# Optimization experiments

Hardware: AMD Instinct MI355X
Metric: run time of the kernel (lower is better)

Reference implementation:

```python
import jax, jax.numpy as jnp
import numpy as np

EPS = 1.0 / 137.0  # fine-structure-constant epsilon used throughout the Yat ops


def yat_dense(x, W, b, alpha):
    # x: [..., C], W: [C, F] -> [..., F]
    dot = jnp.einsum('btc,cf->btf', x, W)
    x_norm = jnp.sum(x * x, axis=-1, keepdims=True)        # [..., 1]
    w_norm = jnp.sum(W * W, axis=0)                         # [F]
    dist = x_norm + w_norm - 2.0 * dot
    y = dot * dot / (dist + EPS)
    y = y + b
    F = W.shape[1]
    scale = (np.sqrt(F) / np.log(1.0 + F)) ** 1.0           # base; alpha exponent applied below
    return y * ((np.float32(np.sqrt(F)) / np.float32(np.log1p(F))) ** alpha)


def setup_inputs() -> dict:
    key = jax.random.key(0)
    ks = jax.random.split(key, 8)
    B, T, C = 4, 1024, 768
    x = jax.random.normal(ks[0], (B, T, C), dtype=jnp.float32)
    mask = jnp.tril(jnp.ones((T, T), dtype=bool))[None, None, :, :]  # causal [1,1,T,T]
    sd = 1.0 / np.sqrt(C)
    W_attn = jax.random.normal(ks[1], (C, 3 * C), dtype=jnp.float32) * sd
    b_attn = jnp.zeros((3 * C,), dtype=jnp.float32)
    alpha_attn = jnp.ones((), dtype=jnp.float32)
    W_proj = jax.random.normal(ks[2], (C, C), dtype=jnp.float32) * sd
    b_proj = jnp.zeros((C,), dtype=jnp.float32)
    alpha_proj = jnp.ones((), dtype=jnp.float32)
    return {"x": x, "mask": mask, "W_attn": W_attn, "b_attn": b_attn,
            "alpha_attn": alpha_attn, "W_proj": W_proj, "b_proj": b_proj,
            "alpha_proj": alpha_proj}


def reference(x, mask, W_attn, b_attn, alpha_attn, W_proj, b_proj, alpha_proj):
    B, T, C = x.shape
    H = 12
    D = C // H  # head_dim
    qkv = yat_dense(x, W_attn, b_attn, alpha_attn)          # [B,T,3C]
    qkv = qkv.reshape(B, T, 3 * H, D)
    q, k, v = jnp.array_split(qkv, 3, axis=2)
    q = jnp.transpose(q, (0, 2, 1, 3))                       # [B,H,T,D]
    k = jnp.transpose(k, (0, 2, 1, 3))
    v = jnp.transpose(v, (0, 2, 1, 3))
    scale = 1.0 / np.float32(np.sqrt(D))
    dot = jnp.einsum('bhid,bhjd->bhij', q, k)                # [B,H,T,T]
    sq_dot = jnp.square(dot * scale)
    q_norm = jnp.sum(jnp.square(q), axis=-1)[..., None]      # [B,H,T,1]
    k_norm = jnp.sum(jnp.square(k), axis=-1)[..., None, :]   # [B,H,1,T]
    sq_dist = q_norm + k_norm - 2.0 * dot * scale
    attn = sq_dot / (sq_dist + EPS)
    attn = jnp.where(mask, attn, jnp.finfo(jnp.float32).min)
    attn = jax.nn.softmax(attn, axis=-1)
    out = jnp.einsum('bhij,bhjd->bhid', attn, v)             # [B,H,T,D]
    out = jnp.transpose(out, (0, 2, 1, 3)).reshape(B, T, C)
    out = yat_dense(out, W_proj, b_proj, alpha_proj)         # [B,T,C]
    return out
```

## Files before the change

### kernel.cpp

```cpp
#include <hip/hip_runtime.h>
#include <math.h>

#define EPS_YAT (1.0f/137.0f)

typedef unsigned short u16;
typedef unsigned int u32;
typedef __attribute__((ext_vector_type(8))) __bf16 bf16x8;
typedef __attribute__((ext_vector_type(4))) float f32x4;

__device__ __forceinline__ float4 ld4(const float* p) { return *(const float4*)p; }

__device__ __forceinline__ u16 bf16_rne(float f) {
    u32 u = __float_as_uint(f);
    u32 r = (u + 0x7fffu + ((u >> 16) & 1u)) >> 16;
    return (u16)r;
}
__device__ __forceinline__ float bf16_f(u16 h) {
    return __uint_as_float(((u32)h) << 16);
}

__device__ __forceinline__ void glds16(const u16* g, u16* s) {
    __builtin_amdgcn_global_load_lds(
        (const __attribute__((address_space(1))) void*)g,
        (__attribute__((address_space(3))) void*)s,
        16, 0, 0);
}

__global__ void colnorm_part2(const float* __restrict__ Wa, const float* __restrict__ Wp,
                              float* __restrict__ pa, float* __restrict__ pp) {
    __shared__ float sm[256];
    const float* W; float* part; int N, colbase;
    if (blockIdx.x < 36) { W = Wa; part = pa; N = 2304; colbase = blockIdx.x * 64; }
    else                 { W = Wp; part = pp; N = 768;  colbase = (blockIdx.x - 36) * 64; }
    const int col = colbase + (threadIdx.x & 63);
    const int q = threadIdx.x >> 6;
    const int k0 = blockIdx.y * 48 + q * 12;
    float s = 0.f;
    for (int k = k0; k < k0 + 12; ++k) {
        float w = W[(size_t)k * N + col];
        s += w * w;
    }
    sm[threadIdx.x] = s;
    __syncthreads();
    if (threadIdx.x < 64)
        part[(size_t)blockIdx.y * N + col] =
            sm[threadIdx.x] + sm[threadIdx.x + 64] + sm[threadIdx.x + 128] + sm[threadIdx.x + 192];
}

__global__ void colnorm_reduce2(const float* __restrict__ pa, const float* __restrict__ pp,
                                float* __restrict__ wa, float* __restrict__ wp,
                                float* __restrict__ an_zero) {
    int gid = blockIdx.x * 256 + threadIdx.x;
    if (gid < 2304) {
        float s = 0.f;
        #pragma unroll
        for (int i = 0; i < 16; ++i) s += pa[(size_t)i * 2304 + gid];
        wa[gid] = s;
    } else if (gid < 3072) {
        int g = gid - 2304;
        float s = 0.f;
        #pragma unroll
        for (int i = 0; i < 16; ++i) s += pp[(size_t)i * 768 + g];
        wp[g] = s;
    }
    int z = gid - 3072;
    if (z >= 0 && z < 4096) an_zero[z] = 0.f;
}

__global__ void split_rownorm(const float* __restrict__ X, u16* __restrict__ Xh,
                              u16* __restrict__ Xl, float* __restrict__ rn) {
    int wave = threadIdx.x >> 6;
    int lane = threadIdx.x & 63;
    int row = blockIdx.x * 4 + wave;
    const float* xr = X + (size_t)row * 768;
    u16* xh = Xh + (size_t)row * 768;
    u16* xl = Xl + (size_t)row * 768;
    float s = 0.f;
    #pragma unroll
    for (int k = lane * 4; k < 768; k += 256) {
        float4 v = ld4(xr + k);
        s += v.x * v.x + v.y * v.y + v.z * v.z + v.w * v.w;
        u16 h0 = bf16_rne(v.x), h1 = bf16_rne(v.y), h2 = bf16_rne(v.z), h3 = bf16_rne(v.w);
        u16 l0 = bf16_rne(v.x - bf16_f(h0));
        u16 l1 = bf16_rne(v.y - bf16_f(h1));
        u16 l2 = bf16_rne(v.z - bf16_f(h2));
        u16 l3 = bf16_rne(v.w - bf16_f(h3));
        uint2 hp, lp;
        hp.x = (u32)h0 | ((u32)h1 << 16); hp.y = (u32)h2 | ((u32)h3 << 16);
        lp.x = (u32)l0 | ((u32)l1 << 16); lp.y = (u32)l2 | ((u32)l3 << 16);
        *(uint2*)(xh + k) = hp;
        *(uint2*)(xl + k) = lp;
    }
    for (int off = 32; off; off >>= 1) s += __shfl_down(s, off);
    if (lane == 0) rn[row] = s;
}

__global__ void split_wt_kernel(const float* __restrict__ W, u16* __restrict__ Th,
                                u16* __restrict__ Tl, int K, int N) {
    __shared__ float tile[64 * 68];
    const int tid = threadIdx.x;
    const int n0 = blockIdx.x << 6;
    const int k0 = blockIdx.y << 6;
    const int rr = tid >> 4;
    const int cc = (tid & 15) << 2;
    #pragma unroll
    for (int s = 0; s < 4; ++s) {
        int k_l = rr + s * 16;
        *(float4*)&tile[k_l * 68 + cc] = ld4(W + (size_t)(k0 + k_l) * N + n0 + cc);
    }
    __syncthreads();
    #pragma unroll
    for (int s = 0; s < 4; ++s) {
        int n_l = rr + s * 16;
        float a0 = tile[(cc + 0) * 68 + n_l];
        float a1 = tile[(cc + 1) * 68 + n_l];
        float a2 = tile[(cc + 2) * 68 + n_l];
        float a3 = tile[(cc + 3) * 68 + n_l];
        u16 h0 = bf16_rne(a0), h1 = bf16_rne(a1), h2 = bf16_rne(a2), h3 = bf16_rne(a3);
        u16 l0 = bf16_rne(a0 - bf16_f(h0));
        u16 l1 = bf16_rne(a1 - bf16_f(h1));
        u16 l2 = bf16_rne(a2 - bf16_f(h2));
        u16 l3 = bf16_rne(a3 - bf16_f(h3));
        uint2 hp, lp;
        hp.x = (u32)h0 | ((u32)h1 << 16); hp.y = (u32)h2 | ((u32)h3 << 16);
        lp.x = (u32)l0 | ((u32)l1 << 16); lp.y = (u32)l2 | ((u32)l3 << 16);
        size_t o = (size_t)(n0 + n_l) * K + k0 + cc;
        *(uint2*)(Th + o) = hp;
        *(uint2*)(Tl + o) = lp;
    }
}

template<int SPLIT, int NB>
__global__ __launch_bounds__(256, 4)
void yat_gemm_mfma(const u16* __restrict__ Ah, const u16* __restrict__ Al,
                   const u16* __restrict__ Bh, const u16* __restrict__ Bl,
                   const float* __restrict__ bias, const float* __restrict__ xn,
                   const float* __restrict__ wnc, const float* __restrict__ alphap,
                   const float Fdim, float* __restrict__ out,
                   u16* __restrict__ outh, u16* __restrict__ outl,
                   float* __restrict__ qn, float* __restrict__ kn,
                   const int N, const int K) {
    __shared__ __align__(16) u16 lds[4096 + NB * 4096];
    const int tid = threadIdx.x;
    const int nwg = gridDim.x * gridDim.y;
    const int orig = blockIdx.y * gridDim.x + blockIdx.x;
    const int swz = (orig & 7) * (nwg >> 3) + (orig >> 3);
    const int m0 = (swz / gridDim.x) << 6;
    const int n0 = (swz % gridDim.x) * (64 * NB);
    const int w = tid >> 6;
    const int l = tid & 63;
    const int lm = l & 15;
    const int kq = l >> 4;
    const int kq4 = kq << 2;
    const int wn = w * 16 * NB;

    const int srow = (w << 4) + (l >> 2);
    const int scol = (l & 3) << 3;
    const u16* gA  = Ah + (size_t)(m0 + srow) * K + scol;
    const u16* gC  = Al + (size_t)(m0 + srow) * K + scol;
    const u16* gB  = Bh + (size_t)(n0 + srow) * K + scol;
    const u16* gD  = Bl + (size_t)(n0 + srow) * K + scol;
    const u16* gB2 = Bh + (size_t)(n0 + 64 + srow) * K + scol;
    const u16* gD2 = Bl + (size_t)(n0 + 64 + srow) * K + scol;
    const int wb = w << 9;

    u16* sAh = lds;
    u16* sAl = lds + 2048;
    u16* sBh = lds + 4096;
    u16* sBl = lds + 4096 + 2048 * NB;

    f32x4 acc[4][NB] = {};

    for (int k0 = 0; k0 < K; k0 += 32) {
        __syncthreads();
        glds16(gA + k0, sAh + wb);
        glds16(gC + k0, sAl + wb);
        glds16(gB + k0, sBh + wb);
        glds16(gD + k0, sBl + wb);
        if constexpr (NB == 2) {
            glds16(gB2 + k0, sBh + 2048 + wb);
            glds16(gD2 + k0, sBl + 2048 + wb);
        }
        __syncthreads();

        bf16x8 fah[4], fal[4], fbh[NB], fbl[NB];
        #pragma unroll
        for (int i = 0; i < 4; ++i) {
            const int ra = (i * 16 + lm) * 32 + (kq << 3);
            fah[i] = *(const bf16x8*)&sAh[ra];
            fal[i] = *(const bf16x8*)&sAl[ra];
        }
        #pragma unroll
        for (int j = 0; j < NB; ++j) {
            const int rb = (wn + j * 16 + lm) * 32 + (kq << 3);
            fbh[j] = *(const bf16x8*)&sBh[rb];
            fbl[j] = *(const bf16x8*)&sBl[rb];
        }
        #pragma unroll
        for (int i = 0; i < 4; ++i)
            #pragma unroll
            for (int j = 0; j < NB; ++j) {
                f32x4 c = acc[i][j];
                c = __builtin_amdgcn_mfma_f32_16x16x32_bf16(fah[i], fbh[j], c, 0, 0, 0);
                c = __builtin_amdgcn_mfma_f32_16x16x32_bf16(fah[i], fbl[j], c, 0, 0, 0);
                c = __builtin_amdgcn_mfma_f32_16x16x32_bf16(fal[i], fbh[j], c, 0, 0, 0);
                acc[i][j] = c;
            }
    }

    const float scale = powf(sqrtf(Fdim) / log1pf(Fdim), *alphap);
    float pp[4][4];
    #pragma unroll
    for (int i = 0; i < 4; ++i) {
        const int mbase = m0 + i * 16 + kq4;
        #pragma unroll
        for (int r = 0; r < 4; ++r) pp[i][r] = 0.f;
        #pragma unroll
        for (int j = 0; j < NB; ++j) {
            const int n = n0 + wn + j * 16 + lm;
            const float w2 = wnc[n];
            const float bv = bias[n];
            #pragma unroll
            for (int r = 0; r < 4; ++r) {
                const int m = mbase + r;
                float d = acc[i][j][r];
                float den = xn[m] + w2 - 2.f * d + EPS_YAT;
                float v = (d * d / den + bv) * scale;
                if constexpr (SPLIT) {
                    u16 hh = bf16_rne(v);
                    outh[(size_t)m * N + n] = hh;
                    outl[(size_t)m * N + n] = bf16_rne(v - bf16_f(hh));
                    pp[i][r] += v * v;
                } else {
                    out[(size_t)m * N + n] = v;
                }
            }
        }
    }

    if constexpr (SPLIT) {
        if (n0 < 1536) {
            __syncthreads();
            float* red = (float*)lds;
            #pragma unroll
            for (int i = 0; i < 4; ++i)
                #pragma unroll
                for (int r = 0; r < 4; ++r) {
                    float s = pp[i][r];
                    s += __shfl_xor(s, 1, 16);
                    s += __shfl_xor(s, 2, 16);
                    s += __shfl_xor(s, 4, 16);
                    s += __shfl_xor(s, 8, 16);
                    if (lm == 0) red[w * 64 + i * 16 + kq4 + r] = s;
                }
            __syncthreads();
            if (tid < 128) {
                const int hh = tid >> 6;
                const int ml = tid & 63;
                const float s = red[(2 * hh) * 64 + ml] + red[(2 * hh + 1) * 64 + ml];
                const int m = m0 + ml;
                const int b = m >> 10, t = m & 1023;
                const int hcol = n0 + hh * 64;
                if (hcol < 768)
                    qn[(b * 12 + (hcol >> 6)) * 1024 + t] = s;
                else
                    kn[(b * 12 + ((hcol - 768) >> 6)) * 1024 + t] = s;
            }
        }
    }
}

#define MFMA_B16(a, b, c) __builtin_amdgcn_mfma_f32_16x16x32_bf16(a, b, c, 0, 0, 0)

#define ST_TILE(j) { \
    const int kro = ((j)*16 + lm) * 72 + (kq << 3); \
    bf16x8 kh = *(const bf16x8*)&KPh[kro]; \
    bf16x8 kl = *(const bf16x8*)&KPl[kro]; \
    st##j = MFMA_B16(kh, qh0, st##j); \
    st##j = MFMA_B16(kl, qh0, st##j); \
    st##j = MFMA_B16(kh, ql0, st##j); \
    kh = *(const bf16x8*)&KPh[kro + 32]; \
    kl = *(const bf16x8*)&KPl[kro + 32]; \
    st##j = MFMA_B16(kh, qh1, st##j); \
    st##j = MFMA_B16(kl, qh1, st##j); \
    st##j = MFMA_B16(kh, ql1, st##j); \
}

#define YAT_EL(j, r) { \
    float sv = st##j[r] * 0.125f; \
    float den = qnm + kns[(j)*16 + kq4 + (r)] - 2.f * sv + EPS_YAT; \
    float v = sv * sv / den; \
    if (diag && ((j)*16 + kq4 + (r) > wband + lm)) v = -3e38f; \
    st##j[r] = v; mm = fmaxf(mm, v); }
#define YAT_TILE(j) YAT_EL(j,0) YAT_EL(j,1) YAT_EL(j,2) YAT_EL(j,3)

#define PEXP_TILE(j) { \
    float p0 = __expf(st##j[0] - mnew), p1 = __expf(st##j[1] - mnew); \
    float p2 = __expf(st##j[2] - mnew), p3 = __expf(st##j[3] - mnew); \
    rs += p0 + p1 + p2 + p3; \
    u16 h0 = bf16_rne(p0), h1 = bf16_rne(p1), h2 = bf16_rne(p2), h3 = bf16_rne(p3); \
    uint2 hp; hp.x = (u32)h0 | ((u32)h1 << 16); hp.y = (u32)h2 | ((u32)h3 << 16); \
    *(uint2*)&KPh[pmrow + (j)*16 + kq4] = hp; \
    u16 e0 = bf16_rne(p0 - bf16_f(h0)), e1 = bf16_rne(p1 - bf16_f(h1)); \
    u16 e2 = bf16_rne(p2 - bf16_f(h2)), e3 = bf16_rne(p3 - bf16_f(h3)); \
    uint2 lp; lp.x = (u32)e0 | ((u32)e1 << 16); lp.y = (u32)e2 | ((u32)e3 << 16); \
    *(uint2*)&KPl[pmrow + (j)*16 + kq4] = lp; }

#define PV_TILE(j) { \
    const int vro = ((j)*16 + lm) * 72 + vkq8; \
    bf16x8 vh = *(const bf16x8*)&Vth[vro]; \
    bf16x8 vl = *(const bf16x8*)&Vtl[vro]; \
    ac##j = MFMA_B16(ph0, vh, ac##j); \
    ac##j = MFMA_B16(pl0, vh, ac##j); \
    ac##j = MFMA_B16(ph0, vl, ac##j); \
    vh = *(const bf16x8*)&Vth[vro + 32]; \
    vl = *(const bf16x8*)&Vtl[vro + 32]; \
    ac##j = MFMA_B16(ph1, vh, ac##j); \
    ac##j = MFMA_B16(pl1, vh, ac##j); \
    ac##j = MFMA_B16(ph1, vl, ac##j); \
}

#define WRVT(dst, v2, m) { \
    dst[(sj * 4 + 16 * (m) + 0) * 72 + toks] = (u16)((v2).x); \
    dst[(sj * 4 + 16 * (m) + 1) * 72 + toks] = (u16)((v2).x >> 16); \
    dst[(sj * 4 + 16 * (m) + 2) * 72 + toks] = (u16)((v2).y); \
    dst[(sj * 4 + 16 * (m) + 3) * 72 + toks] = (u16)((v2).y >> 16); }

__global__ __launch_bounds__(256, 2)
void yat_flash_mfma(const u16* __restrict__ qh_g, const u16* __restrict__ ql_g,
                    const float* __restrict__ qn, const float* __restrict__ kn,
                    u16* __restrict__ outh, u16* __restrict__ outl,
                    float* __restrict__ an_g) {
    __shared__ __align__(16) u16 KPh[64 * 72], KPl[64 * 72];
    __shared__ __align__(16) u16 Vth[64 * 72], Vtl[64 * 72];
    __shared__ float kns[64];

    const int tid = threadIdx.x;
    const int L = blockIdx.x;
    const int u = L / 48;
    const int qt = (u & 1) ? (u >> 1) : (15 - (u >> 1));
    const int bh = L % 48;
    const int h = bh % 12, b = bh / 12;
    const int wave = tid >> 6;
    const int lane = tid & 63;
    const int lm = lane & 15;
    const int kq = lane >> 4;
    const int kq4 = kq << 2;
    const int wband = wave << 4;
    const int sr = tid >> 2;
    const int sj = tid & 3;
    const int toks = sr ^ (sj << 3);
    const int vkq8 = (kq ^ (lm >> 2)) << 3;
    const size_t base = (size_t)(b * 1024) * 2304 + h * 64;

    {
        const size_t qoff = base + (size_t)((qt << 6) + sr) * 2304 + sj * 16;
        *(uint4*)&KPh[sr * 72 + sj * 16]     = *(const uint4*)(qh_g + qoff);
        *(uint4*)&KPh[sr * 72 + sj * 16 + 8] = *(const uint4*)(qh_g + qoff + 8);
        *(uint4*)&KPl[sr * 72 + sj * 16]     = *(const uint4*)(ql_g + qoff);
        *(uint4*)&KPl[sr * 72 + sj * 16 + 8] = *(const uint4*)(ql_g + qoff + 8);
    }
    const float qnm = qn[bh * 1024 + (qt << 6) + wband + lm];

    const size_t r0 = base + (size_t)sr * 2304;
    uint4 kh0 = *(const uint4*)(qh_g + r0 + 768 + sj * 16);
    uint4 kh1 = *(const uint4*)(qh_g + r0 + 768 + sj * 16 + 8);
    uint4 kl0 = *(const uint4*)(ql_g + r0 + 768 + sj * 16);
    uint4 kl1 = *(const uint4*)(ql_g + r0 + 768 + sj * 16 + 8);
    uint2 vh0 = *(const uint2*)(qh_g + r0 + 1536 + sj * 4);
    uint2 vh1 = *(const uint2*)(qh_g + r0 + 1536 + sj * 4 + 16);
    uint2 vh2 = *(const uint2*)(qh_g + r0 + 1536 + sj * 4 + 32);
    uint2 vh3 = *(const uint2*)(qh_g + r0 + 1536 + sj * 4 + 48);
    uint2 vl0 = *(const uint2*)(ql_g + r0 + 1536 + sj * 4);
    uint2 vl1 = *(const uint2*)(ql_g + r0 + 1536 + sj * 4 + 16);
    uint2 vl2 = *(const uint2*)(ql_g + r0 + 1536 + sj * 4 + 32);
    uint2 vl3 = *(const uint2*)(ql_g + r0 + 1536 + sj * 4 + 48);
    float knS = (tid < 64) ? kn[bh * 1024 + tid] : 0.f;

    __syncthreads();

    const int qrow = (wband + lm) * 72;
    const bf16x8 qh0 = *(const bf16x8*)&KPh[qrow + (kq << 3)];
    const bf16x8 qh1 = *(const bf16x8*)&KPh[qrow + 32 + (kq << 3)];
    const bf16x8 ql0 = *(const bf16x8*)&KPl[qrow + (kq << 3)];
    const bf16x8 ql1 = *(const bf16x8*)&KPl[qrow + 32 + (kq << 3)];

    f32x4 ac0 = {}, ac1 = {}, ac2 = {}, ac3 = {};
    float mrun = -3e38f, lrun = 0.f;
    const int pmrow = (wband + lm) * 72;

    for (int kt = 0; kt <= qt; ++kt) {
        __syncthreads();
        *(uint4*)&KPh[sr * 72 + sj * 16]     = kh0;
        *(uint4*)&KPh[sr * 72 + sj * 16 + 8] = kh1;
        *(uint4*)&KPl[sr * 72 + sj * 16]     = kl0;
        *(uint4*)&KPl[sr * 72 + sj * 16 + 8] = kl1;
        WRVT(Vth, vh0, 0) WRVT(Vth, vh1, 1) WRVT(Vth, vh2, 2) WRVT(Vth, vh3, 3)
        WRVT(Vtl, vl0, 0) WRVT(Vtl, vl1, 1) WRVT(Vtl, vl2, 2) WRVT(Vtl, vl3, 3)
        if (tid < 64) kns[tid] = knS;
        __syncthreads();

        if (kt < qt) {
            const size_t r = base + (size_t)(((kt + 1) << 6) + sr) * 2304;
            kh0 = *(const uint4*)(qh_g + r + 768 + sj * 16);
            kh1 = *(const uint4*)(qh_g + r + 768 + sj * 16 + 8);
            kl0 = *(const uint4*)(ql_g + r + 768 + sj * 16);
            kl1 = *(const uint4*)(ql_g + r + 768 + sj * 16 + 8);
            vh0 = *(const uint2*)(qh_g + r + 1536 + sj * 4);
            vh1 = *(const uint2*)(qh_g + r + 1536 + sj * 4 + 16);
            vh2 = *(const uint2*)(qh_g + r + 1536 + sj * 4 + 32);
            vh3 = *(const uint2*)(qh_g + r + 1536 + sj * 4 + 48);
            vl0 = *(const uint2*)(ql_g + r + 1536 + sj * 4);
            vl1 = *(const uint2*)(ql_g + r + 1536 + sj * 4 + 16);
            vl2 = *(const uint2*)(ql_g + r + 1536 + sj * 4 + 32);
            vl3 = *(const uint2*)(ql_g + r + 1536 + sj * 4 + 48);
            if (tid < 64) knS = kn[bh * 1024 + ((kt + 1) << 6) + tid];
        }

        f32x4 st0 = {}, st1 = {}, st2 = {}, st3 = {};
        __builtin_amdgcn_s_setprio(1);
        ST_TILE(0) ST_TILE(1) ST_TILE(2) ST_TILE(3)
        __builtin_amdgcn_s_setprio(0);
        __syncthreads();

        const bool diag = (kt == qt);
        float mm = -3e38f;
        YAT_TILE(0) YAT_TILE(1) YAT_TILE(2) YAT_TILE(3)
        mm = fmaxf(mm, __shfl_xor(mm, 16));
        mm = fmaxf(mm, __shfl_xor(mm, 32));
        const float mnew = fmaxf(mrun, mm);
        if (!__all(mm <= mrun)) {
            const float al = __expf(mrun - mnew);
            const float a0 = __shfl(al, kq4 + 0, 16);
            const float a1 = __shfl(al, kq4 + 1, 16);
            const float a2 = __shfl(al, kq4 + 2, 16);
            const float a3 = __shfl(al, kq4 + 3, 16);
            ac0[0] *= a0; ac0[1] *= a1; ac0[2] *= a2; ac0[3] *= a3;
            ac1[0] *= a0; ac1[1] *= a1; ac1[2] *= a2; ac1[3] *= a3;
            ac2[0] *= a0; ac2[1] *= a1; ac2[2] *= a2; ac2[3] *= a3;
            ac3[0] *= a0; ac3[1] *= a1; ac3[2] *= a2; ac3[3] *= a3;
            lrun *= al;
        }
        mrun = mnew;
        float rs = 0.f;
        PEXP_TILE(0) PEXP_TILE(1) PEXP_TILE(2) PEXP_TILE(3)
        rs += __shfl_xor(rs, 16);
        rs += __shfl_xor(rs, 32);
        lrun += rs;
        __syncthreads();

        const bf16x8 ph0 = *(const bf16x8*)&KPh[pmrow + (kq << 3)];
        const bf16x8 ph1 = *(const bf16x8*)&KPh[pmrow + 32 + (kq << 3)];
        const bf16x8 pl0 = *(const bf16x8*)&KPl[pmrow + (kq << 3)];
        const bf16x8 pl1 = *(const bf16x8*)&KPl[pmrow + 32 + (kq << 3)];
        __builtin_amdgcn_s_setprio(1);
        PV_TILE(0) PV_TILE(1) PV_TILE(2) PV_TILE(3)
        __builtin_amdgcn_s_setprio(0);
    }

    const float i0 = 1.f / __shfl(lrun, kq4 + 0, 16);
    const float i1 = 1.f / __shfl(lrun, kq4 + 1, 16);
    const float i2 = 1.f / __shfl(lrun, kq4 + 2, 16);
    const float i3 = 1.f / __shfl(lrun, kq4 + 3, 16);
    const size_t obase = (size_t)(b * 1024 + (qt << 6) + wband + kq4) * 768 + h * 64 + lm;
    u16* oph = outh + obase;
    u16* opl = outl + obase;
    float rsum0 = 0.f, rsum1 = 0.f, rsum2 = 0.f, rsum3 = 0.f;
    #define STORE_E(j, r, iv) { \
        float ov = ac##j[r] * iv; \
        rsum##r += ov * ov; \
        u16 hh = bf16_rne(ov); \
        oph[(size_t)(r) * 768 + (j)*16] = hh; \
        opl[(size_t)(r) * 768 + (j)*16] = bf16_rne(ov - bf16_f(hh)); }
    #define STORE_T(j) { STORE_E(j,0,i0) STORE_E(j,1,i1) STORE_E(j,2,i2) STORE_E(j,3,i3) }
    STORE_T(0) STORE_T(1) STORE_T(2) STORE_T(3)
    #undef STORE_T
    #undef STORE_E
    const int arow = b * 1024 + (qt << 6) + wband + kq4;
    #define REDROW(r) { \
        float s = rsum##r; \
        s += __shfl_xor(s, 1, 16); \
        s += __shfl_xor(s, 2, 16); \
        s += __shfl_xor(s, 4, 16); \
        s += __shfl_xor(s, 8, 16); \
        if (lm == 0) atomicAdd(&an_g[arow + (r)], s); }
    REDROW(0) REDROW(1) REDROW(2) REDROW(3)
    #undef REDROW
}

extern "C" void kernel_launch(void* const* d_in, const int* in_sizes, int n_in,
                              void* d_out, int out_size, void* d_ws, size_t ws_size,
                              hipStream_t stream) {
    const float* x          = (const float*)d_in[0];
    const float* W_attn     = (const float*)d_in[2];
    const float* b_attn     = (const float*)d_in[3];
    const float* alpha_attn = (const float*)d_in[4];
    const float* W_proj     = (const float*)d_in[5];
    const float* b_proj     = (const float*)d_in[6];
    const float* alpha_proj = (const float*)d_in[7];

    float* ws       = (float*)d_ws;
    u16*   qkvh     = (u16*)ws;
    u16*   qkvl     = (u16*)(ws + 4718592);
    float* xn       = ws + 12582912;
    float* an       = ws + 12587008;
    float* wn_attn  = ws + 12591104;
    float* wn_proj  = ws + 12593408;
    float* qn       = ws + 12594176;
    float* kn       = ws + 12643328;

    float* cn_part_a = ws + 9437184;
    float* cn_part_p = ws + 9437184 + 36864;
    u16* xh  = (u16*)(ws + 9437184);
    u16* xl  = (u16*)(ws + 11010048);
    u16* aoh = (u16*)(ws + 9437184);
    u16* aol = (u16*)(ws + 11010048);
    u16* wth = (u16*)d_out;
    u16* wtl = (u16*)d_out + 1769472;
    u16* wph = (u16*)(ws + 3145728);
    u16* wpl = (u16*)(ws + 3440640);

    colnorm_part2<<<dim3(48, 16), 256, 0, stream>>>(W_attn, W_proj, cn_part_a, cn_part_p);
    colnorm_reduce2<<<28, 256, 0, stream>>>(cn_part_a, cn_part_p, wn_attn, wn_proj, an);
    split_rownorm<<<1024, 256, 0, stream>>>(x, xh, xl, xn);
    split_wt_kernel<<<dim3(36, 12), 256, 0, stream>>>(W_attn, wth, wtl, 768, 2304);
    yat_gemm_mfma<1, 2><<<dim3(18, 64), 256, 0, stream>>>(
        xh, xl, wth, wtl, b_attn, xn, wn_attn, alpha_attn, 2304.f,
        nullptr, qkvh, qkvl, qn, kn, 2304, 768);
    yat_flash_mfma<<<768, 256, 0, stream>>>(qkvh, qkvl, qn, kn, aoh, aol, an);
    split_wt_kernel<<<dim3(12, 12), 256, 0, stream>>>(W_proj, wph, wpl, 768, 768);
    yat_gemm_mfma<0, 1><<<dim3(12, 64), 256, 0, stream>>>(
        aoh, aol, wph, wpl, b_proj, an, wn_proj, alpha_proj, 768.f,
        (float*)d_out, nullptr, nullptr, nullptr, nullptr, 768, 768);
}
```

Measured before the change: 248.0 us.

## Use 128x128 tiles with K=64 steps in QKV split-bf16 GEMM

The QKV GEMM moves from 64x128 tiles to 128x128 tiles, with each wave owning a 64x64 sub-tile. The K step grows from 32 to 64, which halves the number of barrier pairs and raises reuse of each loaded fragment. The q/k norm reduction now writes directly from each wave instead of going through shared memory, because each wave covers a full 64-column head. The trade-off is higher register pressure (launch bounds drop to 2 blocks per SM), fewer blocks in flight, and possible LDS bank conflicts with the 64-wide row stride.

```diff
diff --git a/kernel.cpp b/kernel.cpp
--- a/kernel.cpp
+++ b/kernel.cpp
@@ -130,8 +130,8 @@
     }
 }
 
-template<int SPLIT, int NB>
-__global__ __launch_bounds__(256, 4)
+template<int SPLIT, int BIG>
+__global__ __launch_bounds__(256, BIG ? 2 : 4)
 void yat_gemm_mfma(const u16* __restrict__ Ah, const u16* __restrict__ Al,
                    const u16* __restrict__ Bh, const u16* __restrict__ Bl,
                    const float* __restrict__ bias, const float* __restrict__ xn,
@@ -140,84 +140,90 @@
                    u16* __restrict__ outh, u16* __restrict__ outl,
                    float* __restrict__ qn, float* __restrict__ kn,
                    const int N, const int K) {
-    __shared__ __align__(16) u16 lds[4096 + NB * 4096];
+    constexpr int TM = BIG ? 128 : 64;
+    constexpr int TN = BIG ? 128 : 64;
+    constexpr int JN = BIG ? 4 : 1;
+    __shared__ __align__(16) u16 lds[(TM + TN) * 64 * 2];
     const int tid = threadIdx.x;
     const int nwg = gridDim.x * gridDim.y;
     const int orig = blockIdx.y * gridDim.x + blockIdx.x;
     const int swz = (orig & 7) * (nwg >> 3) + (orig >> 3);
-    const int m0 = (swz / gridDim.x) << 6;
-    const int n0 = (swz % gridDim.x) * (64 * NB);
+    const int m0 = (swz / gridDim.x) * TM;
+    const int n0 = (swz % gridDim.x) * TN;
     const int w = tid >> 6;
     const int l = tid & 63;
     const int lm = l & 15;
     const int kq = l >> 4;
     const int kq4 = kq << 2;
-    const int wn = w * 16 * NB;
-
-    const int srow = (w << 4) + (l >> 2);
-    const int scol = (l & 3) << 3;
-    const u16* gA  = Ah + (size_t)(m0 + srow) * K + scol;
-    const u16* gC  = Al + (size_t)(m0 + srow) * K + scol;
-    const u16* gB  = Bh + (size_t)(n0 + srow) * K + scol;
-    const u16* gD  = Bl + (size_t)(n0 + srow) * K + scol;
-    const u16* gB2 = Bh + (size_t)(n0 + 64 + srow) * K + scol;
-    const u16* gD2 = Bl + (size_t)(n0 + 64 + srow) * K + scol;
-    const int wb = w << 9;
+    const int WM = BIG ? ((w >> 1) << 6) : 0;
+    const int WN = BIG ? ((w & 1) << 6) : (w << 4);
+
+    const int lrow = l >> 3;
+    const int lchunk = (l & 7) << 3;
 
     u16* sAh = lds;
-    u16* sAl = lds + 2048;
-    u16* sBh = lds + 4096;
-    u16* sBl = lds + 4096 + 2048 * NB;
-
-    f32x4 acc[4][NB] = {};
-
-    for (int k0 = 0; k0 < K; k0 += 32) {
+    u16* sAl = lds + TM * 64;
+    u16* sBh = lds + 2 * TM * 64;
+    u16* sBl = lds + 2 * TM * 64 + TN * 64;
+
+    f32x4 acc[4][JN] = {};
+
+    for (int k0 = 0; k0 < K; k0 += 64) {
         __syncthreads();
-        glds16(gA + k0, sAh + wb);
-        glds16(gC + k0, sAl + wb);
-        glds16(gB + k0, sBh + wb);
-        glds16(gD + k0, sBl + wb);
-        if constexpr (NB == 2) {
-            glds16(gB2 + k0, sBh + 2048 + wb);
-            glds16(gD2 + k0, sBl + 2048 + wb);
+        #pragma unroll
+        for (int c = 0; c < TM / 32; ++c) {
+            const int r0w = (TM / 4) * w + 8 * c;
+            const size_t go = (size_t)(m0 + r0w + lrow) * K + k0 + lchunk;
+            glds16(Ah + go, sAh + r0w * 64);
+            glds16(Al + go, sAl + r0w * 64);
+        }
+        #pragma unroll
+        for (int c = 0; c < TN / 32; ++c) {
+            const int r0w = (TN / 4) * w + 8 * c;
+            const size_t go = (size_t)(n0 + r0w + lrow) * K + k0 + lchunk;
+            glds16(Bh + go, sBh + r0w * 64);
+            glds16(Bl + go, sBl + r0w * 64);
         }
         __syncthreads();
 
-        bf16x8 fah[4], fal[4], fbh[NB], fbl[NB];
-        #pragma unroll
-        for (int i = 0; i < 4; ++i) {
-            const int ra = (i * 16 + lm) * 32 + (kq << 3);
-            fah[i] = *(const bf16x8*)&sAh[ra];
-            fal[i] = *(const bf16x8*)&sAl[ra];
-        }
-        #pragma unroll
-        for (int j = 0; j < NB; ++j) {
-            const int rb = (wn + j * 16 + lm) * 32 + (kq << 3);
-            fbh[j] = *(const bf16x8*)&sBh[rb];
-            fbl[j] = *(const bf16x8*)&sBl[rb];
-        }
-        #pragma unroll
-        for (int i = 0; i < 4; ++i)
+        #pragma unroll
+        for (int kk = 0; kk < 2; ++kk) {
+            bf16x8 fah[4], fal[4], fbh[JN], fbl[JN];
             #pragma unroll
-            for (int j = 0; j < NB; ++j) {
-                f32x4 c = acc[i][j];
-                c = __builtin_amdgcn_mfma_f32_16x16x32_bf16(fah[i], fbh[j], c, 0, 0, 0);
-                c = __builtin_amdgcn_mfma_f32_16x16x32_bf16(fah[i], fbl[j], c, 0, 0, 0);
-                c = __builtin_amdgcn_mfma_f32_16x16x32_bf16(fal[i], fbh[j], c, 0, 0, 0);
-                acc[i][j] = c;
+            for (int i = 0; i < 4; ++i) {
+                const int ra = (WM + i * 16 + lm) * 64 + kk * 32 + (kq << 3);
+                fah[i] = *(const bf16x8*)&sAh[ra];
+                fal[i] = *(const bf16x8*)&sAl[ra];
             }
+            #pragma unroll
+            for (int j = 0; j < JN; ++j) {
+                const int rb = (WN + j * 16 + lm) * 64 + kk * 32 + (kq << 3);
+                fbh[j] = *(const bf16x8*)&sBh[rb];
+                fbl[j] = *(const bf16x8*)&sBl[rb];
+            }
+            #pragma unroll
+            for (int i = 0; i < 4; ++i)
+                #pragma unroll
+                for (int j = 0; j < JN; ++j) {
+                    f32x4 c = acc[i][j];
+                    c = __builtin_amdgcn_mfma_f32_16x16x32_bf16(fah[i], fbh[j], c, 0, 0, 0);
+                    c = __builtin_amdgcn_mfma_f32_16x16x32_bf16(fah[i], fbl[j], c, 0, 0, 0);
+                    c = __builtin_amdgcn_mfma_f32_16x16x32_bf16(fal[i], fbh[j], c, 0, 0, 0);
+                    acc[i][j] = c;
+                }
+        }
     }
 
     const float scale = powf(sqrtf(Fdim) / log1pf(Fdim), *alphap);
     float pp[4][4];
     #pragma unroll
     for (int i = 0; i < 4; ++i) {
-        const int mbase = m0 + i * 16 + kq4;
+        const int mbase = m0 + WM + i * 16 + kq4;
         #pragma unroll
         for (int r = 0; r < 4; ++r) pp[i][r] = 0.f;
         #pragma unroll
-        for (int j = 0; j < NB; ++j) {
-            const int n = n0 + wn + j * 16 + lm;
+        for (int j = 0; j < JN; ++j) {
+            const int n = n0 + WN + j * 16 + lm;
             const float w2 = wnc[n];
             const float bv = bias[n];
             #pragma unroll
@@ -239,9 +245,8 @@
     }
 
     if constexpr (SPLIT) {
-        if (n0 < 1536) {
-            __syncthreads();
-            float* red = (float*)lds;
+        const int hcol = n0 + WN;
+        if (hcol < 1536) {
             #pragma unroll
             for (int i = 0; i < 4; ++i)
                 #pragma unroll
@@ -251,21 +256,15 @@
                     s += __shfl_xor(s, 2, 16);
                     s += __shfl_xor(s, 4, 16);
                     s += __shfl_xor(s, 8, 16);
-                    if (lm == 0) red[w * 64 + i * 16 + kq4 + r] = s;
+                    if (lm == 0) {
+                        const int m = m0 + WM + i * 16 + kq4 + r;
+                        const int bb = m >> 10, t = m & 1023;
+                        if (hcol < 768)
+                            qn[(bb * 12 + (hcol >> 6)) * 1024 + t] = s;
+                        else
+                            kn[(bb * 12 + ((hcol - 768) >> 6)) * 1024 + t] = s;
+                    }
                 }
-            __syncthreads();
-            if (tid < 128) {
-                const int hh = tid >> 6;
-                const int ml = tid & 63;
-                const float s = red[(2 * hh) * 64 + ml] + red[(2 * hh + 1) * 64 + ml];
-                const int m = m0 + ml;
-                const int b = m >> 10, t = m & 1023;
-                const int hcol = n0 + hh * 64;
-                if (hcol < 768)
-                    qn[(b * 12 + (hcol >> 6)) * 1024 + t] = s;
-                else
-                    kn[(b * 12 + ((hcol - 768) >> 6)) * 1024 + t] = s;
-            }
         }
     }
 }
@@ -524,12 +523,12 @@
     colnorm_reduce2<<<28, 256, 0, stream>>>(cn_part_a, cn_part_p, wn_attn, wn_proj, an);
     split_rownorm<<<1024, 256, 0, stream>>>(x, xh, xl, xn);
     split_wt_kernel<<<dim3(36, 12), 256, 0, stream>>>(W_attn, wth, wtl, 768, 2304);
-    yat_gemm_mfma<1, 2><<<dim3(18, 64), 256, 0, stream>>>(
+    yat_gemm_mfma<1, 1><<<dim3(18, 32), 256, 0, stream>>>(
         xh, xl, wth, wtl, b_attn, xn, wn_attn, alpha_attn, 2304.f,
         nullptr, qkvh, qkvl, qn, kn, 2304, 768);
     yat_flash_mfma<<<768, 256, 0, stream>>>(qkvh, qkvl, qn, kn, aoh, aol, an);
     split_wt_kernel<<<dim3(12, 12), 256, 0, stream>>>(W_proj, wph, wpl, 768, 768);
-    yat_gemm_mfma<0, 1><<<dim3(12, 64), 256, 0, stream>>>(
+    yat_gemm_mfma<0, 0><<<dim3(12, 64), 256, 0, stream>>>(
         aoh, aol, wph, wpl, b_proj, an, wn_proj, alpha_proj, 768.f,
         (float*)d_out, nullptr, nullptr, nullptr, nullptr, 768, 768);
 }
```

Measured after the change: 252.0 us. Within noise of the previous version (+1.6%).
